# Optimization experiments

Hardware: AMD Instinct MI355X
Metric: run time of the kernel (lower is better)

Reference implementation:

```python
import jax, jax.numpy as jnp
import numpy as np

NUM_HEADS = 12
ROPE_THETA = 10000.0


def _rope_cos_sin(n, hd, dtype):
    inv_freq = 1.0 / (ROPE_THETA ** (np.arange(0, hd, 2, dtype=np.float64) / hd))
    freqs = np.outer(np.arange(n, dtype=np.float64), inv_freq)  # (N, hd/2)
    emb = np.concatenate([freqs, freqs], axis=-1)               # (N, hd)
    return jnp.asarray(np.cos(emb), dtype), jnp.asarray(np.sin(emb), dtype)


def _apply_rope(t, cos, sin):
    # t: (B, H, N, hd); rotate-half convention
    half = t.shape[-1] // 2
    t1, t2 = t[..., :half], t[..., half:]
    rot = jnp.concatenate([-t2, t1], axis=-1)
    return t * cos + rot * sin


def setup_inputs() -> dict:
    key = jax.random.key(0)
    k1, k2, k3 = jax.random.split(key, 3)
    B, N, C = 8, 1024, 768
    x = jax.random.normal(k1, (B, N, C), dtype=jnp.float32)
    w_qkv = jax.random.normal(k2, (C, 3 * C), dtype=jnp.float32) * 0.02
    w_proj = jax.random.normal(k3, (C, C), dtype=jnp.float32) * 0.02
    b_proj = jnp.zeros((C,), dtype=jnp.float32)
    return {"x": x, "w_qkv": w_qkv, "w_proj": w_proj, "b_proj": b_proj}


def reference(x, w_qkv, w_proj, b_proj):
    B, N, C = x.shape
    H = NUM_HEADS
    hd = C // H
    scale = hd ** -0.5
    # qkv: (B,N,3C) -> (B,N,3,H,hd) -> (B,H,3,N,hd)
    qkv = (x @ w_qkv).reshape(B, N, 3, H, hd).transpose(0, 3, 2, 1, 4)
    q, k, v = qkv[:, :, 0], qkv[:, :, 1], qkv[:, :, 2]  # each (B,H,N,hd)
    cos, sin = _rope_cos_sin(N, hd, x.dtype)
    q = _apply_rope(q, cos, sin)
    k = _apply_rope(k, cos, sin)
    attn = jax.nn.softmax(jnp.einsum("bhqd,bhkd->bhqk", q, k) * scale, axis=-1)
    out = jnp.einsum("bhqk,bhkd->bhqd", attn, v)  # (B,H,N,hd)
    out = out.transpose(0, 2, 1, 3).reshape(B, N, C)
    return out @ w_proj + b_proj
```

## Files before the change

### kernel.cpp

```cpp
#include <hip/hip_runtime.h>

typedef unsigned short ushort_t;
typedef __bf16 bf16x8 __attribute__((ext_vector_type(8)));
typedef float f32x4 __attribute__((ext_vector_type(4)));
typedef float f32x16 __attribute__((ext_vector_type(16)));
typedef unsigned short u16x8 __attribute__((ext_vector_type(8)));
typedef unsigned int u32x2 __attribute__((ext_vector_type(2)));
typedef unsigned int u32x4 __attribute__((ext_vector_type(4)));

#define MFMA16(a, b, c) __builtin_amdgcn_mfma_f32_16x16x32_bf16((a), (b), (c), 0, 0, 0)
#define MFMA32(a, b, c) __builtin_amdgcn_mfma_f32_32x32x16_bf16((a), (b), (c), 0, 0, 0)

#define SEQ 1024
#define NHEAD 12
#define HD 64
#define CDIM 768
#define TS 6291456
#define QSCALE 0.1803368801111204f

__device__ __forceinline__ ushort_t f2bf(float f) {
  __bf16 b = (__bf16)f;
  return __builtin_bit_cast(ushort_t, b);
}
__device__ __forceinline__ unsigned pk2(float lo, float hi) {
  return (unsigned)f2bf(lo) | ((unsigned)f2bf(hi) << 16);
}

__device__ __forceinline__ void plswap(unsigned &a, unsigned &b) {
  u32x2 r = __builtin_amdgcn_permlane32_swap(a, b, false, false);
  a = r[0];
  b = r[1];
}

typedef __attribute__((address_space(1))) void gvoid_t;
typedef __attribute__((address_space(3))) void lvoid_t;
__device__ __forceinline__ void async16(const ushort_t* g, ushort_t* l) {
  __builtin_amdgcn_global_load_lds((gvoid_t*)g, (lvoid_t*)l, 16, 0, 0);
}

__device__ __forceinline__ void transpose_body(const float* __restrict__ in,
                                               ushort_t* __restrict__ out,
                                               int R, int C, int bxi, int byi,
                                               float (*tile)[33]) {
  int bx = bxi * 32, by = byi * 32;
  int tx = threadIdx.x & 31, ty = threadIdx.x >> 5;
#pragma unroll
  for (int i = ty; i < 32; i += 8) {
    int r = by + i, c = bx + tx;
    if (r < R && c < C) tile[i][tx] = in[(size_t)r * C + c];
  }
  __syncthreads();
#pragma unroll
  for (int i = ty; i < 32; i += 8) {
    int r = bx + i, c = by + tx;
    if (r < C && c < R) out[(size_t)r * R + c] = f2bf(tile[tx][i]);
  }
}

__global__ void __launch_bounds__(256) prep_all(const float* __restrict__ x,
                                                const float* __restrict__ w_qkv,
                                                const float* __restrict__ w_proj,
                                                ushort_t* __restrict__ xb,
                                                ushort_t* __restrict__ wqkvT,
                                                ushort_t* __restrict__ wprojT,
                                                float* __restrict__ tab) {
  __shared__ float tile[32][33];
  const int bid = blockIdx.x;
  if (bid < 3072) {
    int i = (bid * 256 + threadIdx.x) * 8;
    float4 a = *(const float4*)(x + i);
    float4 b = *(const float4*)(x + i + 4);
    u16x8 r;
    r[0] = f2bf(a.x); r[1] = f2bf(a.y); r[2] = f2bf(a.z); r[3] = f2bf(a.w);
    r[4] = f2bf(b.x); r[5] = f2bf(b.y); r[6] = f2bf(b.z); r[7] = f2bf(b.w);
    *(u16x8*)(xb + i) = r;
  } else if (bid < 3072 + 1728) {
    int t = bid - 3072;
    transpose_body(w_qkv, wqkvT, 768, 2304, t % 72, t / 72, tile);
  } else if (bid < 3072 + 1728 + 576) {
    int t = bid - (3072 + 1728);
    transpose_body(w_proj, wprojT, 768, 768, t % 24, t / 24, tile);
  } else {
    int g = (bid - 5376) * 256 + threadIdx.x;
    int n = g >> 5, j = g & 31;
    double invf = pow(10000.0, -((double)(2 * j)) / 64.0);
    double fr = (double)n * invf;
    tab[g * 2]     = (float)cos(fr);
    tab[g * 2 + 1] = (float)sin(fr);
  }
}

__device__ __forceinline__ void gemm_compute32(const ushort_t* la, const ushort_t* lb,
                                               int wm, int wn, int fr, int fq,
                                               f32x4 acc[4][4]) {
  bf16x8 aF[4], bF[4];
#pragma unroll
  for (int i = 0; i < 4; ++i) {
    const int R = wm + i * 16 + fr;
    aF[i] = *(const bf16x8*)(la + R * 32 + (((fq + (R >> 1)) & 3) << 3));
  }
#pragma unroll
  for (int j = 0; j < 4; ++j) {
    const int S = wn + j * 16 + fr;
    bF[j] = *(const bf16x8*)(lb + S * 32 + (((fq + (S >> 1)) & 3) << 3));
  }
#pragma unroll
  for (int i = 0; i < 4; ++i)
#pragma unroll
    for (int j = 0; j < 4; ++j) acc[i][j] = MFMA16(aF[i], bF[j], acc[i][j]);
}

__device__ __forceinline__ void gemm_bt_core(const ushort_t* __restrict__ A,
                                             const ushort_t* __restrict__ Bt,
                                             int bm, int bn,
                                             ushort_t (*ldsA)[4096],
                                             ushort_t (*ldsB)[4096],
                                             f32x4 acc[4][4]) {
  const int tid = threadIdx.x;
  const int lane = tid & 63, wid = tid >> 6;
  const int wm = (wid >> 1) * 64, wn = (wid & 1) * 64;
  const int fr = lane & 15, fq = lane >> 4;
#pragma unroll
  for (int i = 0; i < 4; ++i)
#pragma unroll
    for (int j = 0; j < 4; ++j) acc[i][j] = (f32x4){0.f, 0.f, 0.f, 0.f};

  const int srow = tid >> 2;
  const int scol = (((tid & 3) - (srow >> 1)) & 3) << 3;
  const ushort_t* aSrc = A + (size_t)(bm + srow) * CDIM + scol;
  const ushort_t* bSrc = Bt + (size_t)(bn + srow) * CDIM + scol;

#define STAGE_STEP(buf, s)                                                       \
  {                                                                              \
    async16(aSrc + (s) * 32, ldsA[buf] + tid * 8);                               \
    async16(aSrc + (size_t)64 * CDIM + (s) * 32, ldsA[buf] + 2048 + tid * 8);    \
    async16(bSrc + (s) * 32, ldsB[buf] + tid * 8);                               \
    async16(bSrc + (size_t)64 * CDIM + (s) * 32, ldsB[buf] + 2048 + tid * 8);    \
  }

  STAGE_STEP(0, 0);
  STAGE_STEP(1, 1);
  STAGE_STEP(2, 2);

#pragma unroll 3
  for (int s = 0; s < 21; ++s) {
    const int b = s % 3;
    asm volatile("s_waitcnt vmcnt(8)" ::: "memory");
    __builtin_amdgcn_sched_barrier(0);
    __builtin_amdgcn_s_barrier();
    __builtin_amdgcn_sched_barrier(0);
    gemm_compute32(ldsA[b], ldsB[b], wm, wn, fr, fq, acc);
    __builtin_amdgcn_sched_barrier(0);
    __builtin_amdgcn_s_barrier();
    __builtin_amdgcn_sched_barrier(0);
    STAGE_STEP(b, s + 3);
  }
  asm volatile("s_waitcnt vmcnt(8)" ::: "memory");
  __builtin_amdgcn_sched_barrier(0);
  __builtin_amdgcn_s_barrier();
  __builtin_amdgcn_sched_barrier(0);
  gemm_compute32(ldsA[0], ldsB[0], wm, wn, fr, fq, acc);
  asm volatile("s_waitcnt vmcnt(4)" ::: "memory");
  __builtin_amdgcn_sched_barrier(0);
  __builtin_amdgcn_s_barrier();
  __builtin_amdgcn_sched_barrier(0);
  gemm_compute32(ldsA[1], ldsB[1], wm, wn, fr, fq, acc);
  asm volatile("s_waitcnt vmcnt(0)" ::: "memory");
  __builtin_amdgcn_sched_barrier(0);
  __builtin_amdgcn_s_barrier();
  __builtin_amdgcn_sched_barrier(0);
  gemm_compute32(ldsA[2], ldsB[2], wm, wn, fr, fq, acc);
#undef STAGE_STEP
}

__global__ void __launch_bounds__(256) gemm_qkv(const ushort_t* __restrict__ A,
                                                const ushort_t* __restrict__ Bt,
                                                const float* __restrict__ tab,
                                                ushort_t* __restrict__ qkv) {
  __shared__ __attribute__((aligned(16))) ushort_t ldsA[3][4096];
  __shared__ __attribute__((aligned(16))) ushort_t ldsB[3][4096];
  f32x4 acc[4][4];
  const int f = blockIdx.x;
  const int xcd = f & 7, r = f >> 3;
  const int bm = (xcd * 8 + (r & 7)) * 128;
  const int bn = (r >> 3) * 128;
  gemm_bt_core(A, Bt, bm, bn, ldsA, ldsB, acc);
  const int lane = threadIdx.x & 63, wid = threadIdx.x >> 6;
  const int wm = (wid >> 1) * 64, wn = (wid & 1) * 64;
  const int fr = lane & 15, fq = lane >> 4;
  const int tensor = bn / 768;

  if (tensor < 2) {
    ushort_t* dstT = qkv + (size_t)tensor * TS;
    const float qs = (tensor == 0) ? QSCALE : 1.0f;
#pragma unroll
    for (int i = 0; i < 4; ++i) {
#pragma unroll
      for (int jp = 0; jp < 2; ++jp) {
        const int col = bn + wn + jp * 16 + fr;
        const int rem = col - tensor * 768;
        const int h = rem >> 6;
        const int d2 = rem & 31;
#pragma unroll
        for (int rr = 0; rr < 4; ++rr) {
          const int row = bm + wm + i * 16 + fq * 4 + rr;
          const int b = row >> 10, n = row & 1023;
          const float2 cs = ((const float2*)tab)[n * 32 + d2];
          const float av = acc[i][jp][rr], bv = acc[i][jp + 2][rr];
          const float o1 = (av * cs.x - bv * cs.y) * qs;
          const float o2 = (bv * cs.x + av * cs.y) * qs;
          ushort_t* dst = dstT + ((size_t)(b * NHEAD + h) * SEQ + n) * HD + d2;
          dst[0]  = f2bf(o1);
          dst[32] = f2bf(o2);
        }
      }
    }
  } else {
    ushort_t* vt = qkv + 2 * (size_t)TS;
#pragma unroll
    for (int i = 0; i < 4; ++i) {
      const int row0 = bm + wm + i * 16 + fq * 4;
      const int b = row0 >> 10, n0 = row0 & 1023;
#pragma unroll
      for (int j = 0; j < 4; ++j) {
        const int col = bn + wn + j * 16 + fr;
        const int rem = col - 1536;
        const int h = rem >> 6, d = rem & 63;
        u32x2 pk;
        pk[0] = pk2(acc[i][j][0], acc[i][j][1]);
        pk[1] = pk2(acc[i][j][2], acc[i][j][3]);
        *(u32x2*)(vt + ((size_t)(b * NHEAD + h) * HD + d) * SEQ + n0) = pk;
      }
    }
  }
}

__global__ void __launch_bounds__(256) gemm_proj(const ushort_t* __restrict__ A,
                                                 const ushort_t* __restrict__ Bt,
                                                 const float* __restrict__ bias,
                                                 float* __restrict__ Cout) {
  __shared__ __attribute__((aligned(16))) ushort_t ldsA[3][4096];
  __shared__ __attribute__((aligned(16))) ushort_t ldsB[3][4096];
  f32x4 acc[4][4];
  const int f = blockIdx.x;
  const int xcd = f & 7, r = f >> 3;
  const int bm = (xcd * 8 + (r & 7)) * 128;
  const int bn = (r >> 3) * 128;
  gemm_bt_core(A, Bt, bm, bn, ldsA, ldsB, acc);
  const int lane = threadIdx.x & 63, wid = threadIdx.x >> 6;
  const int wm = (wid >> 1) * 64, wn = (wid & 1) * 64;
  const int fr = lane & 15, fq = lane >> 4;
#pragma unroll
  for (int i = 0; i < 4; ++i) {
#pragma unroll
    for (int j = 0; j < 4; ++j) {
      const int col = bn + wn + j * 16 + fr;
      const float bv = bias[col];
#pragma unroll
      for (int rr = 0; rr < 4; ++rr) {
        const int row = bm + wm + i * 16 + fq * 4 + rr;
        Cout[(size_t)row * CDIM + col] = acc[i][j][rr] + bv;
      }
    }
  }
}

__global__ void __launch_bounds__(256) attn_fused(const ushort_t* __restrict__ Qb,
                                                  const ushort_t* __restrict__ Kb,
                                                  const ushort_t* __restrict__ VTb,
                                                  ushort_t* __restrict__ Ob) {
  __shared__ __attribute__((aligned(16))) ushort_t ldsK[2][4096];
  __shared__ __attribute__((aligned(16))) ushort_t ldsV[2][4096];

  const int tid = threadIdx.x, lane = tid & 63, wid = tid >> 6;
  const int l31 = lane & 31, h = lane >> 5;

  const int f = blockIdx.x;
  const int xp = f & 7, rest = f >> 3;
  const int g = rest % 12, qb = rest / 12;
  const int head = g * 8 + xp;
  const int q0 = qb * 128;

  const ushort_t* Qh  = Qb  + (size_t)head * (SEQ * HD);
  const ushort_t* Kh  = Kb  + (size_t)head * (SEQ * HD);
  const ushort_t* VTh = VTb + (size_t)head * (HD * SEQ);

  const int qrow = q0 + wid * 32 + l31;
  bf16x8 qF[4];
#pragma unroll
  for (int dk = 0; dk < 4; ++dk)
    qF[dk] = *(const bf16x8*)(Qh + (size_t)qrow * HD + dk * 16 + 8 * h);

  f32x16 ot[2];
#pragma unroll
  for (int dt = 0; dt < 2; ++dt)
#pragma unroll
    for (int i = 0; i < 16; ++i) ot[dt][i] = 0.f;
  float lsum = 0.f;

  const int s0 = tid, s1 = tid + 256;
  const int r0 = s0 >> 3, c0 = ((s0 & 7) - r0) & 7;
  const int r1 = s1 >> 3, c1 = ((s1 & 7) - r1) & 7;

#define ASTAGE(buf, kt)                                                         \
  {                                                                             \
    async16(Kh + (size_t)((kt) * 64 + r0) * HD + c0 * 8, &ldsK[buf][s0 * 8]);   \
    async16(Kh + (size_t)((kt) * 64 + r1) * HD + c1 * 8, &ldsK[buf][s1 * 8]);   \
    async16(VTh + (size_t)r0 * SEQ + (kt) * 64 + c0 * 8, &ldsV[buf][s0 * 8]);   \
    async16(VTh + (size_t)r1 * SEQ + (kt) * 64 + c1 * 8, &ldsV[buf][s1 * 8]);   \
  }

  ASTAGE(0, 0);
  __syncthreads();

  for (int kt = 0; kt < 16; ++kt) {
    const int cur = kt & 1;
    if (kt < 15) ASTAGE(cur ^ 1, kt + 1);

    f32x16 st[2];
    __builtin_amdgcn_s_setprio(1);
#pragma unroll
    for (int ks = 0; ks < 2; ++ks) {
      f32x16 s;
#pragma unroll
      for (int i = 0; i < 16; ++i) s[i] = 0.f;
      const int kr = ks * 32 + l31;
#pragma unroll
      for (int dk = 0; dk < 4; ++dk) {
        const int sw = (dk * 2 + h + kr) & 7;
        bf16x8 kf = *(const bf16x8*)&ldsK[cur][(kr * 8 + sw) * 8];
        s = MFMA32(kf, qF[dk], s);
      }
      st[ks] = s;
    }
    __builtin_amdgcn_s_setprio(0);

    unsigned pk[2][8];
#pragma unroll
    for (int ks = 0; ks < 2; ++ks) {
      float ls = 0.f;
#pragma unroll
      for (int m = 0; m < 8; ++m) {
        const float e0 = __builtin_amdgcn_exp2f(st[ks][2 * m]);
        const float e1 = __builtin_amdgcn_exp2f(st[ks][2 * m + 1]);
        ls += e0 + e1;
        pk[ks][m] = pk2(e0, e1);
      }
      lsum += ls;

#pragma unroll
      for (int kcl = 0; kcl < 2; ++kcl) {
        const int kc = ks * 2 + kcl;
        const int mb = kcl * 4;
        unsigned w0 = pk[ks][mb + 0], w2 = pk[ks][mb + 2];
        unsigned w1 = pk[ks][mb + 1], w3 = pk[ks][mb + 3];
        plswap(w0, w2);
        plswap(w1, w3);
        u32x4 bi;
        bi[0] = w0; bi[1] = w1; bi[2] = w2; bi[3] = w3;
        const bf16x8 pf = __builtin_bit_cast(bf16x8, bi);
        __builtin_amdgcn_s_setprio(1);
#pragma unroll
        for (int dt = 0; dt < 2; ++dt) {
          const int dr = dt * 32 + l31;
          const int sw = (kc * 2 + h + dr) & 7;
          bf16x8 vf = *(const bf16x8*)&ldsV[cur][(dr * 8 + sw) * 8];
          ot[dt] = MFMA32(vf, pf, ot[dt]);
        }
        __builtin_amdgcn_s_setprio(0);
      }
    }
    __syncthreads();
  }
#undef ASTAGE

  lsum += __shfl_xor(lsum, 32);
  const float inv = 1.0f / lsum;
  const int b = head / NHEAD, hh = head - b * NHEAD;
  ushort_t* obase = Ob + ((size_t)(b * SEQ + qrow)) * CDIM + hh * HD;
#pragma unroll
  for (int dt = 0; dt < 2; ++dt) {
#pragma unroll
    for (int r2 = 0; r2 < 4; ++r2) {
      const int d = dt * 32 + 8 * r2 + 4 * h;
      u32x2 w;
      w[0] = pk2(ot[dt][4 * r2 + 0] * inv, ot[dt][4 * r2 + 1] * inv);
      w[1] = pk2(ot[dt][4 * r2 + 2] * inv, ot[dt][4 * r2 + 3] * inv);
      *(u32x2*)(obase + d) = w;
    }
  }
}

extern "C" void kernel_launch(void* const* d_in, const int* in_sizes, int n_in,
                              void* d_out, int out_size, void* d_ws, size_t ws_size,
                              hipStream_t stream) {
  const float* x      = (const float*)d_in[0];
  const float* w_qkv  = (const float*)d_in[1];
  const float* w_proj = (const float*)d_in[2];
  const float* b_proj = (const float*)d_in[3];
  float* out = (float*)d_out;
  char* ws = (char*)d_ws;

  ushort_t* xb     = (ushort_t*)(ws + 0);
  ushort_t* wqkvT  = (ushort_t*)(ws + 12582912);
  ushort_t* wprojT = (ushort_t*)(ws + 16121856);
  ushort_t* qkv    = (ushort_t*)(ws + 17301504);
  float*    tab    = (float*)  (ws + 55050240);
  ushort_t* oattn  = (ushort_t*)(ws + 55312384);

  prep_all<<<5504, 256, 0, stream>>>(x, w_qkv, w_proj, xb, wqkvT, wprojT, tab);
  gemm_qkv<<<1152, 256, 0, stream>>>(xb, wqkvT, tab, qkv);
  attn_fused<<<768, 256, 0, stream>>>(qkv, qkv + TS, qkv + 2 * (size_t)TS, oattn);
  gemm_proj<<<384, 256, 0, stream>>>(oattn, wprojT, b_proj, out);
}
```

Baseline: 194.9 us.

## Widen QKV GEMM tile to 128x256 with inline triple-buffered pipeline

The QKV projection GEMM now computes 128x256 output tiles per block instead of 128x128, halving the grid to 576 blocks. It gets its own inlined 3-stage async LDS pipeline with a doubled B buffer and 32 accumulators per wave, so each loaded A tile is reused across more MFMAs. The RoPE and V-transpose epilogues are extended to the wider tile, and the XCD-aware block mapping is recomputed. The cost is more registers and LDS per block, which may lower occupancy, and fewer blocks than CUs-times-waves to fill the machine.

```diff
diff --git a/kernel.cpp b/kernel.cpp
--- a/kernel.cpp
+++ b/kernel.cpp
@@ -173,21 +173,96 @@
 #undef STAGE_STEP
 }
 
-__global__ void __launch_bounds__(256) gemm_qkv(const ushort_t* __restrict__ A,
-                                                const ushort_t* __restrict__ Bt,
-                                                const float* __restrict__ tab,
-                                                ushort_t* __restrict__ qkv) {
+__global__ void __launch_bounds__(256, 2) gemm_qkv(const ushort_t* __restrict__ A,
+                                                   const ushort_t* __restrict__ Bt,
+                                                   const float* __restrict__ tab,
+                                                   ushort_t* __restrict__ qkv) {
   __shared__ __attribute__((aligned(16))) ushort_t ldsA[3][4096];
-  __shared__ __attribute__((aligned(16))) ushort_t ldsB[3][4096];
-  f32x4 acc[4][4];
+  __shared__ __attribute__((aligned(16))) ushort_t ldsB[3][8192];
+  f32x4 acc[4][8];
+  const int tid = threadIdx.x, lane = tid & 63, wid = tid >> 6;
+  const int wm = (wid >> 1) * 64, wn = (wid & 1) * 128;
+  const int fr = lane & 15, fq = lane >> 4;
+
   const int f = blockIdx.x;
-  const int xcd = f & 7, r = f >> 3;
-  const int bm = (xcd * 8 + (r & 7)) * 128;
-  const int bn = (r >> 3) * 128;
-  gemm_bt_core(A, Bt, bm, bn, ldsA, ldsB, acc);
-  const int lane = threadIdx.x & 63, wid = threadIdx.x >> 6;
-  const int wm = (wid >> 1) * 64, wn = (wid & 1) * 64;
-  const int fr = lane & 15, fq = lane >> 4;
+  const int id = (f & 7) * 72 + (f >> 3);
+  const int mt = id & 63, nt = id >> 6;
+  const int bm = mt * 128, bn = nt * 256;
+
+#pragma unroll
+  for (int i = 0; i < 4; ++i)
+#pragma unroll
+    for (int j = 0; j < 8; ++j) acc[i][j] = (f32x4){0.f, 0.f, 0.f, 0.f};
+
+  const int srow = tid >> 2;
+  const int scol = (((tid & 3) - (srow >> 1)) & 3) << 3;
+  const ushort_t* aSrc = A + (size_t)(bm + srow) * CDIM + scol;
+  const ushort_t* bSrc = Bt + (size_t)(bn + srow) * CDIM + scol;
+
+#define STG(buf, s)                                                              \
+  {                                                                              \
+    async16(aSrc + (s) * 32, ldsA[buf] + tid * 8);                               \
+    async16(aSrc + (size_t)64 * CDIM + (s) * 32, ldsA[buf] + 2048 + tid * 8);    \
+    async16(bSrc + (s) * 32, ldsB[buf] + tid * 8);                               \
+    async16(bSrc + (size_t)64 * CDIM + (s) * 32, ldsB[buf] + 2048 + tid * 8);    \
+    async16(bSrc + (size_t)128 * CDIM + (s) * 32, ldsB[buf] + 4096 + tid * 8);   \
+    async16(bSrc + (size_t)192 * CDIM + (s) * 32, ldsB[buf] + 6144 + tid * 8);   \
+  }
+
+  const int ch = ((fq + (fr >> 1)) & 3) << 3;
+
+  STG(0, 0);
+  STG(1, 1);
+  STG(2, 2);
+
+#pragma unroll 3
+  for (int s = 0; s < 21; ++s) {
+    const int b = s % 3;
+    asm volatile("s_waitcnt vmcnt(12)" ::: "memory");
+    __builtin_amdgcn_sched_barrier(0);
+    __builtin_amdgcn_s_barrier();
+    __builtin_amdgcn_sched_barrier(0);
+    {
+      bf16x8 aF[4], bF[8];
+#pragma unroll
+      for (int i = 0; i < 4; ++i)
+        aF[i] = *(const bf16x8*)(ldsA[b] + (wm + i * 16 + fr) * 32 + ch);
+#pragma unroll
+      for (int j = 0; j < 8; ++j)
+        bF[j] = *(const bf16x8*)(ldsB[b] + (wn + j * 16 + fr) * 32 + ch);
+#pragma unroll
+      for (int i = 0; i < 4; ++i)
+#pragma unroll
+        for (int j = 0; j < 8; ++j) acc[i][j] = MFMA16(aF[i], bF[j], acc[i][j]);
+    }
+    __builtin_amdgcn_sched_barrier(0);
+    __builtin_amdgcn_s_barrier();
+    __builtin_amdgcn_sched_barrier(0);
+    STG(b, s + 3);
+  }
+#pragma unroll
+  for (int t = 0; t < 3; ++t) {
+    if (t == 0) asm volatile("s_waitcnt vmcnt(12)" ::: "memory");
+    else if (t == 1) asm volatile("s_waitcnt vmcnt(6)" ::: "memory");
+    else asm volatile("s_waitcnt vmcnt(0)" ::: "memory");
+    __builtin_amdgcn_sched_barrier(0);
+    __builtin_amdgcn_s_barrier();
+    __builtin_amdgcn_sched_barrier(0);
+    bf16x8 aF[4], bF[8];
+#pragma unroll
+    for (int i = 0; i < 4; ++i)
+      aF[i] = *(const bf16x8*)(ldsA[t] + (wm + i * 16 + fr) * 32 + ch);
+#pragma unroll
+    for (int j = 0; j < 8; ++j)
+      bF[j] = *(const bf16x8*)(ldsB[t] + (wn + j * 16 + fr) * 32 + ch);
+#pragma unroll
+    for (int i = 0; i < 4; ++i)
+#pragma unroll
+      for (int j = 0; j < 8; ++j) acc[i][j] = MFMA16(aF[i], bF[j], acc[i][j]);
+    if (t < 2) { __builtin_amdgcn_s_barrier(); }
+  }
+#undef STG
+
   const int tensor = bn / 768;
 
   if (tensor < 2) {
@@ -196,22 +271,25 @@
 #pragma unroll
     for (int i = 0; i < 4; ++i) {
 #pragma unroll
-      for (int jp = 0; jp < 2; ++jp) {
-        const int col = bn + wn + jp * 16 + fr;
-        const int rem = col - tensor * 768;
-        const int h = rem >> 6;
-        const int d2 = rem & 31;
-#pragma unroll
-        for (int rr = 0; rr < 4; ++rr) {
-          const int row = bm + wm + i * 16 + fq * 4 + rr;
-          const int b = row >> 10, n = row & 1023;
-          const float2 cs = ((const float2*)tab)[n * 32 + d2];
-          const float av = acc[i][jp][rr], bv = acc[i][jp + 2][rr];
-          const float o1 = (av * cs.x - bv * cs.y) * qs;
-          const float o2 = (bv * cs.x + av * cs.y) * qs;
-          ushort_t* dst = dstT + ((size_t)(b * NHEAD + h) * SEQ + n) * HD + d2;
-          dst[0]  = f2bf(o1);
-          dst[32] = f2bf(o2);
+      for (int jg = 0; jg < 2; ++jg) {
+#pragma unroll
+        for (int jp = 0; jp < 2; ++jp) {
+          const int col = bn + wn + jg * 64 + jp * 16 + fr;
+          const int rem = col - tensor * 768;
+          const int h = rem >> 6;
+          const int d2 = rem & 31;
+#pragma unroll
+          for (int rr = 0; rr < 4; ++rr) {
+            const int row = bm + wm + i * 16 + fq * 4 + rr;
+            const int b = row >> 10, n = row & 1023;
+            const float2 cs = ((const float2*)tab)[n * 32 + d2];
+            const float av = acc[i][jg * 4 + jp][rr], bv = acc[i][jg * 4 + jp + 2][rr];
+            const float o1 = (av * cs.x - bv * cs.y) * qs;
+            const float o2 = (bv * cs.x + av * cs.y) * qs;
+            ushort_t* dst = dstT + ((size_t)(b * NHEAD + h) * SEQ + n) * HD + d2;
+            dst[0]  = f2bf(o1);
+            dst[32] = f2bf(o2);
+          }
         }
       }
     }
@@ -222,7 +300,7 @@
       const int row0 = bm + wm + i * 16 + fq * 4;
       const int b = row0 >> 10, n0 = row0 & 1023;
 #pragma unroll
-      for (int j = 0; j < 4; ++j) {
+      for (int j = 0; j < 8; ++j) {
         const int col = bn + wn + j * 16 + fr;
         const int rem = col - 1536;
         const int h = rem >> 6, d = rem & 63;
@@ -409,7 +487,7 @@
   ushort_t* oattn  = (ushort_t*)(ws + 55312384);
 
   prep_all<<<5504, 256, 0, stream>>>(x, w_qkv, w_proj, xb, wqkvT, wprojT, tab);
-  gemm_qkv<<<1152, 256, 0, stream>>>(xb, wqkvT, tab, qkv);
+  gemm_qkv<<<576, 256, 0, stream>>>(xb, wqkvT, tab, qkv);
   attn_fused<<<768, 256, 0, stream>>>(qkv, qkv + TS, qkv + 2 * (size_t)TS, oattn);
   gemm_proj<<<384, 256, 0, stream>>>(oattn, wprojT, b_proj, out);
 }
```

New measurement: 201.2 us. 1.03x slower.
